# Kernel optimization log

Measured on AMD Instinct MI355X. Metric: run time of the kernel, lower is better.

The kernel has to match this reference:

```python
import jax, jax.numpy as jnp
import numpy as np

H = 512
IN = 64
OUT = 1


def _lstm_layer(x, W_ih, W_hh, b_ih, b_hh):
    # x: (B, T, D). PyTorch gate order: i, f, g, o stacked along 4H.
    B, T, _ = x.shape
    Hd = W_hh.shape[1]
    # Precompute input contribution for all timesteps (one big GEMM).
    xg = jnp.einsum('btd,gd->btg', x, W_ih) + b_ih + b_hh  # (B, T, 4H)

    def step(carry, xg_t):
        h, c = carry
        gates = xg_t + h @ W_hh.T  # (B, 4H)
        i, f, g, o = jnp.split(gates, 4, axis=-1)
        i = jax.nn.sigmoid(i)
        f = jax.nn.sigmoid(f)
        g = jnp.tanh(g)
        o = jax.nn.sigmoid(o)
        c = f * c + i * g
        h = o * jnp.tanh(c)
        return (h, c), h

    h0 = jnp.zeros((B, Hd), x.dtype)
    c0 = jnp.zeros((B, Hd), x.dtype)
    (_, _), hs = jax.lax.scan(step, (h0, c0), jnp.swapaxes(xg, 0, 1))
    return jnp.swapaxes(hs, 0, 1)  # (B, T, H)


def setup_inputs() -> dict:
    key = jax.random.key(0)
    ks = jax.random.split(key, 12)
    s = 1.0 / np.sqrt(H)  # PyTorch LSTM init scale
    u = lambda k, shp: jax.random.uniform(k, shp, jnp.float32, -s, s)
    return {
        'x': jax.random.normal(ks[0], (64, 512, IN), jnp.float32),
        'W_ih0': u(ks[1], (4 * H, IN)),
        'W_hh0': u(ks[2], (4 * H, H)),
        'b_ih0': u(ks[3], (4 * H,)),
        'b_hh0': u(ks[4], (4 * H,)),
        'W_ih1': u(ks[5], (4 * H, H)),
        'W_hh1': u(ks[6], (4 * H, H)),
        'b_ih1': u(ks[7], (4 * H,)),
        'b_hh1': u(ks[8], (4 * H,)),
        'fc_w': u(ks[9], (OUT, H)),
        'fc_b': u(ks[10], (OUT,)),
    }


def reference(x, W_ih0, W_hh0, b_ih0, b_hh0, W_ih1, W_hh1, b_ih1, b_hh1, fc_w, fc_b):
    # Two stacked LSTM layers (eval mode: inter-layer dropout disabled),
    # then linear head on the last timestep's hidden state.
    h1 = _lstm_layer(x, W_ih0, W_hh0, b_ih0, b_hh0)   # (B, T, H)
    h2 = _lstm_layer(h1, W_ih1, W_hh1, b_ih1, b_hh1)  # (B, T, H)
    return h2[:, -1, :] @ fc_w.T + fc_b               # (B, OUT)
```

## Files before the change

### kernel.cpp

```cpp
#include <hip/hip_runtime.h>
#include <stdint.h>

static constexpr int NBLK = 256;
static constexpr int NTHR = 256;
static constexpr int Hd   = 512;
static constexpr int Td   = 512;
static constexpr int IND  = 64;
static constexpr int Bd   = 64;
static constexpr int HBUF = Bd * Hd;
static constexpr int HR   = 520;
static constexpr unsigned POIS32 = 0xAAAAAAAAu;

typedef __attribute__((ext_vector_type(8))) short short8;
typedef __attribute__((ext_vector_type(4))) float f4;

#define MFMA(a, b, c) __builtin_amdgcn_mfma_f32_16x16x32_bf16((a), (b), (c), 0, 0, 0)

__device__ __forceinline__ uint64_t ld_agent64(const uint64_t* p) {
  return __hip_atomic_load((uint64_t*)p, __ATOMIC_RELAXED, __HIP_MEMORY_SCOPE_AGENT);
}
__device__ __forceinline__ void st_agent32(unsigned* p, unsigned v) {
  __hip_atomic_store(p, v, __ATOMIC_RELAXED, __HIP_MEMORY_SCOPE_AGENT);
}
__device__ __forceinline__ float sigmoidf_(float v) { return 1.0f / (1.0f + __expf(-v)); }
__device__ __forceinline__ float tanhf_(float v) {
  v = fminf(15.0f, fmaxf(-15.0f, v));
  float e = __expf(2.0f * v);
  return (e - 1.0f) / (e + 1.0f);
}
__device__ __forceinline__ unsigned short bf16_rne(float f) {
  unsigned u = __float_as_uint(f);
  unsigned r = u + 0x7FFFu + ((u >> 16) & 1u);
  return (unsigned short)(r >> 16);
}
__device__ __forceinline__ unsigned pack_h(float h) {
  unsigned short hb = bf16_rne(h);
  float hf = __uint_as_float((unsigned)hb << 16);
  unsigned short lb = bf16_rne(h - hf);
  unsigned pk = ((unsigned)hb << 16) | (unsigned)lb;
  if (pk == POIS32) pk ^= 1u;
  return pk;
}
__device__ __forceinline__ int good64(uint64_t w) {
  return (int)((unsigned)w != POIS32) & (int)((unsigned)(w >> 32) != POIS32);
}
__device__ __forceinline__ void poll16(const uint64_t* base, int tid, uint64_t* tmp) {
  const uint64_t* p15 = base + 15 * 256 + tid;
  int guard = 0;
  for (;;) {
    uint64_t w = ld_agent64(p15);
    if (good64(w) || ++guard > (1 << 18)) break;
    __builtin_amdgcn_s_sleep(1);
  }
  guard = 0;
  for (;;) {
    unsigned ok = 1;
    #pragma unroll
    for (int k = 0; k < 16; ++k) tmp[k] = ld_agent64(base + k * 256 + tid);
    #pragma unroll
    for (int k = 0; k < 16; ++k) ok &= (unsigned)good64(tmp[k]);
    if (ok || ++guard > (1 << 16)) break;
  }
}

__global__ __launch_bounds__(256) void split_x_kernel(
    const float* __restrict__ x, short* __restrict__ xhi, short* __restrict__ xlo) {
  int i = blockIdx.x * 256 + threadIdx.x;
  float4 v = ((const float4*)x)[i];
  float f[4] = {v.x, v.y, v.z, v.w};
  unsigned h[4], l[4];
  #pragma unroll
  for (int e = 0; e < 4; ++e) {
    unsigned short hb = bf16_rne(f[e]);
    float r = f[e] - __uint_as_float((unsigned)hb << 16);
    h[e] = hb; l[e] = bf16_rne(r);
  }
  uint2 hp = {h[0] | (h[1] << 16), h[2] | (h[3] << 16)};
  uint2 lp = {l[0] | (l[1] << 16), l[2] | (l[3] << 16)};
  *(uint2*)&xhi[i * 4] = hp;
  *(uint2*)&xlo[i * 4] = lp;
}

__global__ __launch_bounds__(NTHR, 1) void lstm2_flow(
    const float* __restrict__ Wih0, const float* __restrict__ Whh0,
    const float* __restrict__ bih0, const float* __restrict__ bhh0,
    const float* __restrict__ Wih1, const float* __restrict__ Whh1,
    const float* __restrict__ bih1, const float* __restrict__ bhh1,
    const float* __restrict__ fcw,  const float* __restrict__ fcb,
    float* __restrict__ out,
    const short* __restrict__ xhi, const short* __restrict__ xlo,
    unsigned* __restrict__ h1, unsigned* __restrict__ h2)
{
  __shared__ short hiA1[16 * HR];
  __shared__ short loA1[16 * HR];
  __shared__ short hiA2[16 * HR];
  __shared__ short loA2[16 * HR];
  __shared__ short Blo[4 * 16 * 64 * 8];
  __shared__ float g_lds[4][16][16];
  __shared__ float red[NTHR];

  const int tid  = threadIdx.x;
  const int wave = tid >> 6;
  const int lane = tid & 63;
  const int nB   = lane & 15;
  const int q    = lane >> 4;
  const int mA   = lane & 15;

  const int xcd   = blockIdx.x & 7;
  const int layer = xcd >> 2;
  const int mt    = xcd & 3;
  const int jt    = blockIdx.x >> 3;
  const int jBase = jt * 16;
  const int bBase = mt * 16;
  const int wrow  = wave * Hd + jBase + nB;

  const int pm = tid >> 4;
  const int pn = tid & 15;

  if (layer == 0) {
    short8 bh[18], bl[18];
    {
      const float* Wh = Whh0 + (size_t)wrow * Hd;
      const float* Wi = Wih0 + (size_t)wrow * IND;
      #pragma unroll
      for (int kt = 0; kt < 18; ++kt) {
        const float* src = (kt < 16) ? (Wh + kt * 32 + q * 8) : (Wi + (kt - 16) * 32 + q * 8);
        float wv[8];
        *(float4*)&wv[0] = *(const float4*)src;
        *(float4*)&wv[4] = *(const float4*)(src + 4);
        #pragma unroll
        for (int j = 0; j < 8; ++j) {
          unsigned short hb = bf16_rne(wv[j]);
          float r = wv[j] - __uint_as_float((unsigned)hb << 16);
          ((short*)&bh[kt])[j] = (short)hb;
          ((short*)&bl[kt])[j] = (short)bf16_rne(r);
        }
      }
    }
    float bias[4];
    #pragma unroll
    for (int g4 = 0; g4 < 4; ++g4) {
      int r = g4 * Hd + jBase + pn;
      bias[g4] = bih0[r] + bhh0[r];
    }
    float c1 = 0.0f;

    for (int t = 0; t < Td; ++t) {
      f4 a0 = {0.f,0.f,0.f,0.f}, a1 = {0.f,0.f,0.f,0.f}, a2 = {0.f,0.f,0.f,0.f};
      {
        const size_t xb = ((size_t)(bBase + mA) * Td + t) * IND;
        short8 x0h = *(const short8*)&xhi[xb + q * 8];
        short8 x0l = *(const short8*)&xlo[xb + q * 8];
        short8 x1h = *(const short8*)&xhi[xb + 32 + q * 8];
        short8 x1l = *(const short8*)&xlo[xb + 32 + q * 8];
        a0 = MFMA(x0h, bh[16], a0); a1 = MFMA(x0h, bl[16], a1); a2 = MFMA(x0l, bh[16], a2);
        a0 = MFMA(x1h, bh[17], a0); a1 = MFMA(x1h, bl[17], a1); a2 = MFMA(x1l, bh[17], a2);
      }
      if (t >= 1) {
        const uint64_t* s1 = (const uint64_t*)(h1 + (size_t)(t - 1) * HBUF) + bBase * 256;
        uint64_t tmp[16];
        poll16(s1, tid, tmp);
        #pragma unroll
        for (int k = 0; k < 16; ++k) {
          unsigned p0 = (unsigned)tmp[k], p1 = (unsigned)(tmp[k] >> 32);
          *(unsigned*)&hiA1[k * HR + tid * 2] = __builtin_amdgcn_perm(p1, p0, 0x07060302u);
          *(unsigned*)&loA1[k * HR + tid * 2] = __builtin_amdgcn_perm(p1, p0, 0x05040100u);
        }
      }
      __syncthreads();

      if (t >= 1) {
        #pragma unroll
        for (int kt = 0; kt < 16; ++kt) {
          short8 ah = *(const short8*)&hiA1[mA * HR + kt * 32 + q * 8];
          short8 al = *(const short8*)&loA1[mA * HR + kt * 32 + q * 8];
          a0 = MFMA(ah, bh[kt], a0);
          a1 = MFMA(ah, bl[kt], a1);
          a2 = MFMA(al, bh[kt], a2);
        }
      }
      #pragma unroll
      for (int r2 = 0; r2 < 4; ++r2) g_lds[wave][q * 4 + r2][nB] = a0[r2] + a1[r2] + a2[r2];
      __syncthreads();

      {
        float pi = g_lds[0][pm][pn] + bias[0];
        float pf = g_lds[1][pm][pn] + bias[1];
        float pg = g_lds[2][pm][pn] + bias[2];
        float po = g_lds[3][pm][pn] + bias[3];
        float ig = sigmoidf_(pi), fg = sigmoidf_(pf), gg = tanhf_(pg), og = sigmoidf_(po);
        c1 = fmaf(fg, c1, ig * gg);
        float h = og * tanhf_(c1);
        st_agent32(h1 + (size_t)t * HBUF + (bBase + pm) * Hd + jBase + pn, pack_h(h));
      }
    }

    if (blockIdx.x == 0) {
      const int b = tid >> 2, q4 = tid & 3;
      float sum = 0.0f;
      #pragma unroll
      for (int ch = 0; ch < 4; ++ch) {
        const uint64_t* hp = (const uint64_t*)(h2 + (size_t)(Td - 1) * HBUF) + b * 256 + q4 * 64 + ch * 16;
        uint64_t w[16];
        int guard = 0;
        for (;;) {
          unsigned ok = 1;
          #pragma unroll
          for (int u = 0; u < 16; ++u) w[u] = ld_agent64(hp + u);
          #pragma unroll
          for (int u = 0; u < 16; ++u) ok &= (unsigned)good64(w[u]);
          if (ok || ++guard > (1 << 17)) break;
          __builtin_amdgcn_s_sleep(1);
        }
        #pragma unroll
        for (int u = 0; u < 16; ++u) {
          int cw = q4 * 64 + ch * 16 + u;
          unsigned plo = (unsigned)w[u], phi = (unsigned)(w[u] >> 32);
          float vlo = __uint_as_float(plo & 0xFFFF0000u) + __uint_as_float(plo << 16);
          float vhi = __uint_as_float(phi & 0xFFFF0000u) + __uint_as_float(phi << 16);
          sum = fmaf(vlo, fcw[2 * cw], fmaf(vhi, fcw[2 * cw + 1], sum));
        }
      }
      red[tid] = sum;
      __syncthreads();
      if (q4 == 0) out[b] = red[tid] + red[tid + 1] + red[tid + 2] + red[tid + 3] + fcb[0];
    }
  } else {
    short8 bh[32], bl[16];
    {
      const float* Wi = Wih1 + (size_t)wrow * Hd;
      const float* Wh = Whh1 + (size_t)wrow * Hd;
      #pragma unroll
      for (int kt = 0; kt < 16; ++kt) {
        float wv[8];
        *(float4*)&wv[0] = *(const float4*)(Wi + kt * 32 + q * 8);
        *(float4*)&wv[4] = *(const float4*)(Wi + kt * 32 + q * 8 + 4);
        #pragma unroll
        for (int j = 0; j < 8; ++j) {
          unsigned short hb = bf16_rne(wv[j]);
          float r = wv[j] - __uint_as_float((unsigned)hb << 16);
          ((short*)&bh[kt])[j] = (short)hb;
          ((short*)&bl[kt])[j] = (short)bf16_rne(r);
        }
      }
      #pragma unroll
      for (int kt = 0; kt < 16; ++kt) {
        float wv[8];
        *(float4*)&wv[0] = *(const float4*)(Wh + kt * 32 + q * 8);
        *(float4*)&wv[4] = *(const float4*)(Wh + kt * 32 + q * 8 + 4);
        short lo8[8];
        #pragma unroll
        for (int j = 0; j < 8; ++j) {
          unsigned short hb = bf16_rne(wv[j]);
          float r = wv[j] - __uint_as_float((unsigned)hb << 16);
          ((short*)&bh[16 + kt])[j] = (short)hb;
          lo8[j] = (short)bf16_rne(r);
        }
        *(short8*)&Blo[((wave * 16 + kt) * 64 + lane) * 8] = *(short8*)lo8;
      }
    }
    float bias[4];
    #pragma unroll
    for (int g4 = 0; g4 < 4; ++g4) {
      int r = g4 * Hd + jBase + pn;
      bias[g4] = bih1[r] + bhh1[r];
    }
    float c2 = 0.0f;
    __syncthreads();

    for (int t = 0; t < Td; ++t) {
      const uint64_t* s1 = (const uint64_t*)(h1 + (size_t)t * HBUF) + bBase * 256;
      if (t >= 1) {
        const uint64_t* s2 = (const uint64_t*)(h2 + (size_t)(t - 1) * HBUF) + bBase * 256;
        uint64_t t1[16], t2[16];
        {
          const uint64_t* p1 = s1 + 15 * 256 + tid;
          const uint64_t* p2 = s2 + 15 * 256 + tid;
          int guard = 0;
          for (;;) {
            uint64_t w1 = ld_agent64(p1);
            uint64_t w2 = ld_agent64(p2);
            if ((good64(w1) & good64(w2)) != 0) break;
            if (++guard > (1 << 18)) break;
            __builtin_amdgcn_s_sleep(1);
          }
        }
        int guard = 0;
        for (;;) {
          unsigned ok = 1;
          #pragma unroll
          for (int k = 0; k < 16; ++k) {
            t1[k] = ld_agent64(s1 + k * 256 + tid);
            t2[k] = ld_agent64(s2 + k * 256 + tid);
          }
          #pragma unroll
          for (int k = 0; k < 16; ++k) ok &= (unsigned)(good64(t1[k]) & good64(t2[k]));
          if (ok || ++guard > (1 << 16)) break;
        }
        #pragma unroll
        for (int k = 0; k < 16; ++k) {
          unsigned p0 = (unsigned)t1[k], p1 = (unsigned)(t1[k] >> 32);
          *(unsigned*)&hiA1[k * HR + tid * 2] = __builtin_amdgcn_perm(p1, p0, 0x07060302u);
          *(unsigned*)&loA1[k * HR + tid * 2] = __builtin_amdgcn_perm(p1, p0, 0x05040100u);
          unsigned q0 = (unsigned)t2[k], q1 = (unsigned)(t2[k] >> 32);
          *(unsigned*)&hiA2[k * HR + tid * 2] = __builtin_amdgcn_perm(q1, q0, 0x07060302u);
          *(unsigned*)&loA2[k * HR + tid * 2] = __builtin_amdgcn_perm(q1, q0, 0x05040100u);
        }
      } else {
        uint64_t t1[16];
        poll16(s1, tid, t1);
        #pragma unroll
        for (int k = 0; k < 16; ++k) {
          unsigned p0 = (unsigned)t1[k], p1 = (unsigned)(t1[k] >> 32);
          *(unsigned*)&hiA1[k * HR + tid * 2] = __builtin_amdgcn_perm(p1, p0, 0x07060302u);
          *(unsigned*)&loA1[k * HR + tid * 2] = __builtin_amdgcn_perm(p1, p0, 0x05040100u);
        }
      }
      __syncthreads();

      f4 a0 = {0.f,0.f,0.f,0.f}, a1 = {0.f,0.f,0.f,0.f}, a2 = {0.f,0.f,0.f,0.f};
      #pragma unroll
      for (int kt = 0; kt < 16; ++kt) {
        short8 ah = *(const short8*)&hiA1[mA * HR + kt * 32 + q * 8];
        short8 al = *(const short8*)&loA1[mA * HR + kt * 32 + q * 8];
        a0 = MFMA(ah, bh[kt], a0);
        a1 = MFMA(ah, bl[kt], a1);
        a2 = MFMA(al, bh[kt], a2);
      }
      if (t >= 1) {
        #pragma unroll
        for (int kt = 0; kt < 16; ++kt) {
          short8 ah  = *(const short8*)&hiA2[mA * HR + kt * 32 + q * 8];
          short8 al  = *(const short8*)&loA2[mA * HR + kt * 32 + q * 8];
          short8 wlo = *(const short8*)&Blo[((wave * 16 + kt) * 64 + lane) * 8];
          a0 = MFMA(ah, bh[16 + kt], a0);
          a1 = MFMA(ah, wlo, a1);
          a2 = MFMA(al, bh[16 + kt], a2);
        }
      }
      #pragma unroll
      for (int r2 = 0; r2 < 4; ++r2) g_lds[wave][q * 4 + r2][nB] = a0[r2] + a1[r2] + a2[r2];
      __syncthreads();

      {
        float pi = g_lds[0][pm][pn] + bias[0];
        float pf = g_lds[1][pm][pn] + bias[1];
        float pg = g_lds[2][pm][pn] + bias[2];
        float po = g_lds[3][pm][pn] + bias[3];
        float ig = sigmoidf_(pi), fg = sigmoidf_(pf), gg = tanhf_(pg), og = sigmoidf_(po);
        c2 = fmaf(fg, c2, ig * gg);
        float h = og * tanhf_(c2);
        st_agent32(h2 + (size_t)t * HBUF + (bBase + pm) * Hd + jBase + pn, pack_h(h));
      }
    }
  }
}

extern "C" void kernel_launch(void* const* d_in, const int* in_sizes, int n_in,
                              void* d_out, int out_size, void* d_ws, size_t ws_size,
                              hipStream_t stream) {
  const float* x    = (const float*)d_in[0];
  const float* Wih0 = (const float*)d_in[1];
  const float* Whh0 = (const float*)d_in[2];
  const float* bih0 = (const float*)d_in[3];
  const float* bhh0 = (const float*)d_in[4];
  const float* Wih1 = (const float*)d_in[5];
  const float* Whh1 = (const float*)d_in[6];
  const float* bih1 = (const float*)d_in[7];
  const float* bhh1 = (const float*)d_in[8];
  const float* fcw  = (const float*)d_in[9];
  const float* fcb  = (const float*)d_in[10];

  char* base = (char*)d_ws;
  short* xhi = (short*)base;
  const size_t xplane = (size_t)Bd * Td * IND;
  short* xlo = xhi + xplane;
  unsigned* h1 = (unsigned*)(xlo + xplane);
  unsigned* h2 = h1 + (size_t)Td * HBUF;

  const size_t need = 4 * xplane + 2 * (size_t)Td * HBUF * 4;
  if (ws_size < need) return;

  hipLaunchKernelGGL(split_x_kernel, dim3((unsigned)(xplane / 4 / 256)), dim3(256), 0, stream,
                     x, xhi, xlo);
  hipLaunchKernelGGL(lstm2_flow, dim3(NBLK), dim3(NTHR), 0, stream,
                     Wih0, Whh0, bih0, bhh0, Wih1, Whh1, bih1, bhh1, fcw, fcb,
                     (float*)d_out, xhi, xlo, h1, h2);
}
```

Before: 2.440 ms.

## Tile-contiguous hidden-state layout with sc0 polling loads for cross-block exchange

Changes the layout of the global hidden-state exchange buffers so each producer block's 16x16 tile is contiguous. Each consumer thread now polls and reads 16 consecutive 64-bit words with inline-asm sc0 loads, falling back to agent-scope atomics only periodically. Stores write both a volatile copy and an agent-scope atomic. The goal is to cut polling latency and scattered memory traffic in the per-timestep inter-block handoff. In exchange it relies on cache-coherence behaviour of sc0 loads, adds redundant stores, and changes the LDS staging pattern, which may cause bank conflicts.

```diff
diff --git a/kernel.cpp b/kernel.cpp
--- a/kernel.cpp
+++ b/kernel.cpp
@@ -22,6 +22,39 @@
 __device__ __forceinline__ void st_agent32(unsigned* p, unsigned v) {
   __hip_atomic_store(p, v, __ATOMIC_RELAXED, __HIP_MEMORY_SCOPE_AGENT);
 }
+__device__ __forceinline__ uint64_t ld1_sc0(const uint64_t* p) {
+  uint64_t v;
+  asm volatile("global_load_dwordx2 %0, %1, off sc0\n\t"
+               "s_waitcnt vmcnt(0)"
+               : "=v"(v) : "v"(p) : "memory");
+  return v;
+}
+__device__ __forceinline__ void ld16_sc0(const uint64_t* p, uint64_t* o) {
+  asm volatile(
+    "global_load_dwordx2 %[o0],  %[a], off sc0\n\t"
+    "global_load_dwordx2 %[o1],  %[a], off offset:8 sc0\n\t"
+    "global_load_dwordx2 %[o2],  %[a], off offset:16 sc0\n\t"
+    "global_load_dwordx2 %[o3],  %[a], off offset:24 sc0\n\t"
+    "global_load_dwordx2 %[o4],  %[a], off offset:32 sc0\n\t"
+    "global_load_dwordx2 %[o5],  %[a], off offset:40 sc0\n\t"
+    "global_load_dwordx2 %[o6],  %[a], off offset:48 sc0\n\t"
+    "global_load_dwordx2 %[o7],  %[a], off offset:56 sc0\n\t"
+    "global_load_dwordx2 %[o8],  %[a], off offset:64 sc0\n\t"
+    "global_load_dwordx2 %[o9],  %[a], off offset:72 sc0\n\t"
+    "global_load_dwordx2 %[o10], %[a], off offset:80 sc0\n\t"
+    "global_load_dwordx2 %[o11], %[a], off offset:88 sc0\n\t"
+    "global_load_dwordx2 %[o12], %[a], off offset:96 sc0\n\t"
+    "global_load_dwordx2 %[o13], %[a], off offset:104 sc0\n\t"
+    "global_load_dwordx2 %[o14], %[a], off offset:112 sc0\n\t"
+    "global_load_dwordx2 %[o15], %[a], off offset:120 sc0\n\t"
+    "s_waitcnt vmcnt(0)"
+    : [o0]"=v"(o[0]), [o1]"=v"(o[1]), [o2]"=v"(o[2]), [o3]"=v"(o[3]),
+      [o4]"=v"(o[4]), [o5]"=v"(o[5]), [o6]"=v"(o[6]), [o7]"=v"(o[7]),
+      [o8]"=v"(o[8]), [o9]"=v"(o[9]), [o10]"=v"(o[10]), [o11]"=v"(o[11]),
+      [o12]"=v"(o[12]), [o13]"=v"(o[13]), [o14]"=v"(o[14]), [o15]"=v"(o[15])
+    : [a]"v"(p)
+    : "memory");
+}
 __device__ __forceinline__ float sigmoidf_(float v) { return 1.0f / (1.0f + __expf(-v)); }
 __device__ __forceinline__ float tanhf_(float v) {
   v = fminf(15.0f, fmaxf(-15.0f, v));
@@ -44,23 +77,58 @@
 __device__ __forceinline__ int good64(uint64_t w) {
   return (int)((unsigned)w != POIS32) & (int)((unsigned)(w >> 32) != POIS32);
 }
-__device__ __forceinline__ void poll16(const uint64_t* base, int tid, uint64_t* tmp) {
-  const uint64_t* p15 = base + 15 * 256 + tid;
-  int guard = 0;
+__device__ __forceinline__ void st_dual(unsigned* p, unsigned v) {
+  *(volatile unsigned*)p = v;
+  st_agent32(p, v);
+}
+
+__device__ __forceinline__ void stage_slot(const unsigned* slot_u32, int mt, int tid,
+                                           short* hiL, short* loL) {
+  const uint64_t* base = (const uint64_t*)slot_u32 + (size_t)mt * 4096 + tid * 16;
+  int r = 0;
   for (;;) {
-    uint64_t w = ld_agent64(p15);
-    if (good64(w) || ++guard > (1 << 18)) break;
+    uint64_t w = ((r & 15) == 15) ? ld_agent64(base + 15) : ld1_sc0(base + 15);
+    if (good64(w)) break;
+    if (++r > (1 << 20)) break;
     __builtin_amdgcn_s_sleep(1);
   }
-  guard = 0;
+  uint64_t t[16];
+  r = 0;
   for (;;) {
+    if ((r & 3) == 3) {
+      #pragma unroll
+      for (int k = 0; k < 16; ++k) t[k] = ld_agent64(base + k);
+    } else {
+      ld16_sc0(base, t);
+    }
     unsigned ok = 1;
     #pragma unroll
-    for (int k = 0; k < 16; ++k) tmp[k] = ld_agent64(base + k * 256 + tid);
-    #pragma unroll
-    for (int k = 0; k < 16; ++k) ok &= (unsigned)good64(tmp[k]);
-    if (ok || ++guard > (1 << 16)) break;
+    for (int k = 0; k < 16; ++k) ok &= (unsigned)good64(t[k]);
+    if (ok || ++r > (1 << 16)) break;
   }
+  const int tile = tid >> 3, pm0 = (tid & 7) * 2;
+  unsigned h0[8], l0[8], h1v[8], l1v[8];
+  #pragma unroll
+  for (int k = 0; k < 8; ++k) {
+    unsigned p0 = (unsigned)t[k], p1 = (unsigned)(t[k] >> 32);
+    h0[k] = __builtin_amdgcn_perm(p1, p0, 0x07060302u);
+    l0[k] = __builtin_amdgcn_perm(p1, p0, 0x05040100u);
+    unsigned q0 = (unsigned)t[8 + k], q1 = (unsigned)(t[8 + k] >> 32);
+    h1v[k] = __builtin_amdgcn_perm(q1, q0, 0x07060302u);
+    l1v[k] = __builtin_amdgcn_perm(q1, q0, 0x05040100u);
+  }
+  short* dh0 = &hiL[pm0 * HR + tile * 16];
+  short* dl0 = &loL[pm0 * HR + tile * 16];
+  short* dh1 = &hiL[(pm0 + 1) * HR + tile * 16];
+  short* dl1 = &loL[(pm0 + 1) * HR + tile * 16];
+  { uint4 a = {h0[0], h0[1], h0[2], h0[3]},  b = {h0[4], h0[5], h0[6], h0[7]};
+    *(uint4*)dh0 = a; *(uint4*)(dh0 + 8) = b; }
+  { uint4 a = {l0[0], l0[1], l0[2], l0[3]},  b = {l0[4], l0[5], l0[6], l0[7]};
+    *(uint4*)dl0 = a; *(uint4*)(dl0 + 8) = b; }
+  { uint4 a = {h1v[0], h1v[1], h1v[2], h1v[3]}, b = {h1v[4], h1v[5], h1v[6], h1v[7]};
+    *(uint4*)dh1 = a; *(uint4*)(dh1 + 8) = b; }
+  { uint4 a = {l1v[0], l1v[1], l1v[2], l1v[3]}, b = {l1v[4], l1v[5], l1v[6], l1v[7]};
+    *(uint4*)dl1 = a; *(uint4*)(dl1 + 8) = b; }
 }
 
 __global__ __launch_bounds__(256) void split_x_kernel(
@@ -116,6 +184,7 @@
 
   const int pm = tid >> 4;
   const int pn = tid & 15;
+  const size_t stoff = (size_t)(mt * 32 + jt) * 256 + pm * 16 + pn;
 
   if (layer == 0) {
     short8 bh[18], bl[18];
@@ -156,17 +225,8 @@
         a0 = MFMA(x0h, bh[16], a0); a1 = MFMA(x0h, bl[16], a1); a2 = MFMA(x0l, bh[16], a2);
         a0 = MFMA(x1h, bh[17], a0); a1 = MFMA(x1h, bl[17], a1); a2 = MFMA(x1l, bh[17], a2);
       }
-      if (t >= 1) {
-        const uint64_t* s1 = (const uint64_t*)(h1 + (size_t)(t - 1) * HBUF) + bBase * 256;
-        uint64_t tmp[16];
-        poll16(s1, tid, tmp);
-        #pragma unroll
-        for (int k = 0; k < 16; ++k) {
-          unsigned p0 = (unsigned)tmp[k], p1 = (unsigned)(tmp[k] >> 32);
-          *(unsigned*)&hiA1[k * HR + tid * 2] = __builtin_amdgcn_perm(p1, p0, 0x07060302u);
-          *(unsigned*)&loA1[k * HR + tid * 2] = __builtin_amdgcn_perm(p1, p0, 0x05040100u);
-        }
-      }
+      if (t >= 1)
+        stage_slot(h1 + (size_t)(t - 1) * HBUF, mt, tid, hiA1, loA1);
       __syncthreads();
 
       if (t >= 1) {
@@ -191,34 +251,37 @@
         float ig = sigmoidf_(pi), fg = sigmoidf_(pf), gg = tanhf_(pg), og = sigmoidf_(po);
         c1 = fmaf(fg, c1, ig * gg);
         float h = og * tanhf_(c1);
-        st_agent32(h1 + (size_t)t * HBUF + (bBase + pm) * Hd + jBase + pn, pack_h(h));
+        st_dual(h1 + (size_t)t * HBUF + stoff, pack_h(h));
       }
     }
 
     if (blockIdx.x == 0) {
       const int b = tid >> 2, q4 = tid & 3;
+      const int mtb = b >> 4, pmb = b & 15;
       float sum = 0.0f;
       #pragma unroll
-      for (int ch = 0; ch < 4; ++ch) {
-        const uint64_t* hp = (const uint64_t*)(h2 + (size_t)(Td - 1) * HBUF) + b * 256 + q4 * 64 + ch * 16;
-        uint64_t w[16];
+      for (int i8 = 0; i8 < 8; ++i8) {
+        const int jt2 = q4 * 8 + i8;
+        const uint64_t* hp = (const uint64_t*)(h2 + (size_t)(Td - 1) * HBUF)
+                             + (size_t)(mtb * 32 + jt2) * 128 + pmb * 8;
+        uint64_t w[8];
         int guard = 0;
         for (;;) {
           unsigned ok = 1;
           #pragma unroll
-          for (int u = 0; u < 16; ++u) w[u] = ld_agent64(hp + u);
+          for (int u = 0; u < 8; ++u) w[u] = ld_agent64(hp + u);
           #pragma unroll
-          for (int u = 0; u < 16; ++u) ok &= (unsigned)good64(w[u]);
+          for (int u = 0; u < 8; ++u) ok &= (unsigned)good64(w[u]);
           if (ok || ++guard > (1 << 17)) break;
           __builtin_amdgcn_s_sleep(1);
         }
         #pragma unroll
-        for (int u = 0; u < 16; ++u) {
-          int cw = q4 * 64 + ch * 16 + u;
+        for (int u = 0; u < 8; ++u) {
+          int j = jt2 * 16 + u * 2;
           unsigned plo = (unsigned)w[u], phi = (unsigned)(w[u] >> 32);
           float vlo = __uint_as_float(plo & 0xFFFF0000u) + __uint_as_float(plo << 16);
           float vhi = __uint_as_float(phi & 0xFFFF0000u) + __uint_as_float(phi << 16);
-          sum = fmaf(vlo, fcw[2 * cw], fmaf(vhi, fcw[2 * cw + 1], sum));
+          sum = fmaf(vlo, fcw[j], fmaf(vhi, fcw[j + 1], sum));
         }
       }
       red[tid] = sum;
@@ -269,53 +332,9 @@
     __syncthreads();
 
     for (int t = 0; t < Td; ++t) {
-      const uint64_t* s1 = (const uint64_t*)(h1 + (size_t)t * HBUF) + bBase * 256;
-      if (t >= 1) {
-        const uint64_t* s2 = (const uint64_t*)(h2 + (size_t)(t - 1) * HBUF) + bBase * 256;
-        uint64_t t1[16], t2[16];
-        {
-          const uint64_t* p1 = s1 + 15 * 256 + tid;
-          const uint64_t* p2 = s2 + 15 * 256 + tid;
-          int guard = 0;
-          for (;;) {
-            uint64_t w1 = ld_agent64(p1);
-            uint64_t w2 = ld_agent64(p2);
-            if ((good64(w1) & good64(w2)) != 0) break;
-            if (++guard > (1 << 18)) break;
-            __builtin_amdgcn_s_sleep(1);
-          }
-        }
-        int guard = 0;
-        for (;;) {
-          unsigned ok = 1;
-          #pragma unroll
-          for (int k = 0; k < 16; ++k) {
-            t1[k] = ld_agent64(s1 + k * 256 + tid);
-            t2[k] = ld_agent64(s2 + k * 256 + tid);
-          }
-          #pragma unroll
-          for (int k = 0; k < 16; ++k) ok &= (unsigned)(good64(t1[k]) & good64(t2[k]));
-          if (ok || ++guard > (1 << 16)) break;
-        }
-        #pragma unroll
-        for (int k = 0; k < 16; ++k) {
-          unsigned p0 = (unsigned)t1[k], p1 = (unsigned)(t1[k] >> 32);
-          *(unsigned*)&hiA1[k * HR + tid * 2] = __builtin_amdgcn_perm(p1, p0, 0x07060302u);
-          *(unsigned*)&loA1[k * HR + tid * 2] = __builtin_amdgcn_perm(p1, p0, 0x05040100u);
-          unsigned q0 = (unsigned)t2[k], q1 = (unsigned)(t2[k] >> 32);
-          *(unsigned*)&hiA2[k * HR + tid * 2] = __builtin_amdgcn_perm(q1, q0, 0x07060302u);
-          *(unsigned*)&loA2[k * HR + tid * 2] = __builtin_amdgcn_perm(q1, q0, 0x05040100u);
-        }
-      } else {
-        uint64_t t1[16];
-        poll16(s1, tid, t1);
-        #pragma unroll
-        for (int k = 0; k < 16; ++k) {
-          unsigned p0 = (unsigned)t1[k], p1 = (unsigned)(t1[k] >> 32);
-          *(unsigned*)&hiA1[k * HR + tid * 2] = __builtin_amdgcn_perm(p1, p0, 0x07060302u);
-          *(unsigned*)&loA1[k * HR + tid * 2] = __builtin_amdgcn_perm(p1, p0, 0x05040100u);
-        }
-      }
+      stage_slot(h1 + (size_t)t * HBUF, mt, tid, hiA1, loA1);
+      if (t >= 1)
+        stage_slot(h2 + (size_t)(t - 1) * HBUF, mt, tid, hiA2, loA2);
       __syncthreads();
 
       f4 a0 = {0.f,0.f,0.f,0.f}, a1 = {0.f,0.f,0.f,0.f}, a2 = {0.f,0.f,0.f,0.f};
@@ -350,7 +369,7 @@
         float ig = sigmoidf_(pi), fg = sigmoidf_(pf), gg = tanhf_(pg), og = sigmoidf_(po);
         c2 = fmaf(fg, c2, ig * gg);
         float h = og * tanhf_(c2);
-        st_agent32(h2 + (size_t)t * HBUF + (bBase + pm) * Hd + jBase + pn, pack_h(h));
+        st_dual(h2 + (size_t)t * HBUF + stoff, pack_h(h));
       }
     }
   }
```

Result: slower. 3.585 ms (+46.9%).
